# Kernel tuning notes

Hardware: AMD Instinct MI355X
Metric: run time of the kernel (lower is better)

Reference implementation:

```python
import jax, jax.numpy as jnp
import numpy as np

B, C, H, W = 32, 3, 512, 512
EPS = 1e-8


def _radius_bins(h, w):
    cy, cx = h // 2, w // 2
    y = jnp.arange(h, dtype=jnp.float32) - cy
    x = jnp.arange(w, dtype=jnp.float32) - cx
    radius = jnp.sqrt(y[:, None] ** 2 + x[None, :] ** 2)  # [H, W]
    max_r = min(cy, cx)
    bins = jnp.floor(radius).astype(jnp.int32)
    # pixels with radius >= max_r fall outside all bins in the original loop;
    # route them to a dummy overflow bin that we drop afterwards.
    bins = jnp.where(bins < max_r, bins, max_r)
    return bins.reshape(-1), max_r


def _psd(x):
    f = jnp.fft.fft2(x)                  # over last two dims, like torch.fft.fft2
    psd = jnp.abs(f) ** 2
    return jnp.log(psd + EPS)            # log_power=True


def _radial_average(psd):
    b, c, h, w = psd.shape
    bins, max_r = _radius_bins(h, w)     # [H*W], static
    data = psd.reshape(b * c, h * w).T   # [H*W, B*C]
    sums = jax.ops.segment_sum(data, bins, num_segments=max_r + 1)
    counts = jax.ops.segment_sum(jnp.ones((h * w,), psd.dtype), bins,
                                 num_segments=max_r + 1)
    avg = jnp.where(counts[:, None] > 0, sums / counts[:, None], 0.0)
    avg = avg[:max_r]                    # drop overflow bin -> [max_r, B*C]
    return avg.T.reshape(b, c, max_r)


def setup_inputs() -> dict:
    key = jax.random.key(0)
    k1, k2 = jax.random.split(key)
    predicted = jax.random.normal(k1, (B, C, H, W), dtype=jnp.float32)
    target = jax.random.normal(k2, (B, C, H, W), dtype=jnp.float32)
    return {"predicted": predicted, "target": target}


def reference(predicted, target):
    pred_rad = _radial_average(_psd(predicted))
    targ_rad = _radial_average(_psd(target))
    return jnp.mean(jnp.abs(pred_rad - targ_rad))  # l1, reduction='mean'
```

## Files before the change

kernel.cpp:

```cpp
#include <hip/hip_runtime.h>
#include <math.h>

#define HH 512
#define WW 512
#define IMG (HH*WW)
#define NIMG_PER 96
#define NIMG 192
#define NBIN 256
#define EPSV 1e-8f
#define LN2F 0.69314718055994530942f

#define CSTR 264
#define IMGC (512*CSTR)
#define NT16 17
#define SLOT 575

typedef float v2f  __attribute__((ext_vector_type(2)));
typedef _Float16 h2f __attribute__((ext_vector_type(2)));

__device__ __forceinline__ int drev(int s) {
    return ((s & 7) << 6) | (s & 56) | (s >> 6);
}
__device__ __forceinline__ int fsw(int a) { return a + (a >> 3); }

__device__ __forceinline__ v2f cmul(v2f a, v2f b) {
    return (v2f){a.x, a.x} * b + (v2f){a.y, a.y} * (v2f){-b.y, b.x};
}
__device__ __forceinline__ v2f cni(v2f a) { return (v2f){a.y, -a.x}; }

__device__ __forceinline__ v2f h2tof(unsigned int u) {
    h2f h = __builtin_bit_cast(h2f, u);
    return (v2f){(float)h.x, (float)h.y};
}
__device__ __forceinline__ unsigned int ftoh2(v2f v) {
    return __builtin_bit_cast(unsigned int, __builtin_amdgcn_cvt_pkrtz(v.x, v.y));
}

__device__ __forceinline__ void wsync() {
    asm volatile("" ::: "memory");
    __builtin_amdgcn_wave_barrier();
    asm volatile("" ::: "memory");
}

__device__ __forceinline__ void bfly8(v2f x[8]) {
    const float R = 0.70710678118654752440f;
    v2f t0=x[0]+x[4], t4=x[0]-x[4];
    v2f t1=x[1]+x[5], t5=x[1]-x[5];
    v2f t2=x[2]+x[6], t6=x[2]-x[6];
    v2f t3=x[3]+x[7], t7=x[3]-x[7];
    v2f u0=t0+t2, u2=t0-t2;
    v2f u1=t1+t3, u3=t1-t3;
    x[0]=u0+u1; x[4]=u0-u1;
    { v2f n3 = cni(u3); x[2]=u2+n3; x[6]=u2-n3; }
    v2f s1 = (v2f){R, R} * ((v2f){t5.x, t5.y} + (v2f){t5.y, -t5.x});
    v2f s2 = cni(t6);
    v2f s3 = (v2f){R, R} * ((v2f){t7.y, -t7.x} - (v2f){t7.x, t7.y});
    v2f v0=t4+s2, v2_=t4-s2;
    v2f v1=s1+s3, v3=s1-s3;
    x[1]=v0+v1; x[5]=v0-v1;
    { v2f m3 = cni(v3); x[3]=v2_+m3; x[7]=v2_-m3; }
}

__device__ __forceinline__ void twiddle7(v2f* x, float ang) {
    const float sn = __sinf(ang), cs = __cosf(ang);
    const v2f w1 = (v2f){cs, sn};
    const v2f w2 = cmul(w1, w1);
    const v2f w3 = cmul(w2, w1);
    const v2f w4 = cmul(w2, w2);
    const v2f w5 = cmul(w2, w3);
    const v2f w6 = cmul(w3, w3);
    const v2f w7 = cmul(w3, w4);
    x[1]=cmul(x[1],w1); x[2]=cmul(x[2],w2); x[3]=cmul(x[3],w3);
    x[4]=cmul(x[4],w4); x[5]=cmul(x[5],w5); x[6]=cmul(x[6],w6);
    x[7]=cmul(x[7],w7);
}

__global__ __launch_bounds__(512) void rowfft_kernel(
    const float* __restrict__ pred, const float* __restrict__ targ,
    unsigned int* __restrict__ out, int img_base)
{
    __shared__ v2f sd[8*SLOT];
    const int t    = threadIdx.x;
    const int lane = t & 63;
    const int w    = t >> 6;

    const int pb = blockIdx.x;
    const int li = blockIdx.y;
    const int g  = img_base + li;
    const float* img = (g < NIMG_PER) ? (pred + (size_t)g * IMG)
                                      : (targ + (size_t)(g - NIMG_PER) * IMG);
    const float* rowA = img + (size_t)(pb*16 + 2*w) * WW + lane;
    const float* rowB = rowA + WW;

    v2f* p = sd + w * SLOT;
    v2f x[8];
    const int i = lane;

    #pragma unroll
    for (int j = 0; j < 8; ++j)
        x[j] = (v2f){rowA[64*j], rowB[64*j]};
    bfly8(x);
    twiddle7(x, -0.012271846303085130f * (float)i);
    {
        v2f* q = p + fsw(i);
        #pragma unroll
        for (int j = 0; j < 8; ++j) q[72*j] = x[j];
    }
    wsync();

    {
        v2f* q = p + 72*(i >> 3) + (i & 7);
        #pragma unroll
        for (int j = 0; j < 8; ++j) x[j] = q[9*j];
        bfly8(x);
        twiddle7(x, -0.098174770424681038f * (float)(i & 7));
        #pragma unroll
        for (int j = 0; j < 8; ++j) q[9*j] = x[j];
    }
    wsync();

    {
        v2f* q = p + 9*i;
        #pragma unroll
        for (int j = 0; j < 8; ++j) x[j] = q[j];
        bfly8(x);
        #pragma unroll
        for (int j = 0; j < 8; ++j) q[j] = x[j];
    }
    wsync();

    unsigned int* dstA = out + (size_t)li * IMGC + (size_t)(pb*16 + 2*w) * CSTR;
    unsigned int* dstB = dstA + CSTR;
    #pragma unroll
    for (int it = 0; it < 5; ++it) {
        const int k = it*64 + lane;
        if (k <= 256) {
            const v2f P = p[fsw(drev(k))];
            const v2f Q = p[fsw(drev((512 - k) & 511))];
            const v2f Fa = (v2f){0.5f, 0.5f} * (P + (v2f){Q.x, -Q.y});
            const v2f Fb = (v2f){0.5f, 0.5f} * ((v2f){P.y, -P.x} + (v2f){Q.y, Q.x});
            dstA[k] = ftoh2(Fa);
            dstB[k] = ftoh2(Fb);
        } else if (k < CSTR) {
            dstA[k] = 0u;
            dstB[k] = 0u;
        }
    }
}

__global__ __launch_bounds__(512) void colfft_kernel(
    const unsigned int* __restrict__ in, float* __restrict__ bins2, int img_base)
{
    __shared__ unsigned int sd[16*SLOT];
    __shared__ float bs[4*257];
    const int t    = threadIdx.x;
    const int lane = t & 63;
    const int w    = t >> 6;

    for (int id = t; id < 4*257; id += 512) bs[id] = 0.0f;

    const int li = blockIdx.y;
    const int x0 = blockIdx.x * 16;
    {
        const int y0 = t >> 2;
        const int c  = t & 3;
        int cb = x0 + 4*c;
        if (cb > CSTR - 4) cb = CSTR - 4;
        const uint4* gsrc = (const uint4*)(in + (size_t)li * IMGC
                                              + (size_t)y0 * CSTR + cb);
        unsigned int* d0 = sd + (4*c + 0)*SLOT + fsw(y0);
        unsigned int* d1 = d0 + SLOT;
        unsigned int* d2 = d1 + SLOT;
        unsigned int* d3 = d2 + SLOT;
        #pragma unroll
        for (int it = 0; it < 4; ++it) {
            const uint4 v = gsrc[(size_t)it * 128 * (CSTR/4)];
            d0[144*it] = v.x; d1[144*it] = v.y;
            d2[144*it] = v.z; d3[144*it] = v.w;
        }
    }
    __syncthreads();

    unsigned int* pA = sd + (2*w)     * SLOT;
    unsigned int* pB = sd + (2*w + 1) * SLOT;
    v2f a[8], b[8];
    const int i = lane;

    {
        unsigned int* qA = pA + fsw(i);
        unsigned int* qB = pB + fsw(i);
        #pragma unroll
        for (int j = 0; j < 8; ++j) { a[j] = h2tof(qA[72*j]); b[j] = h2tof(qB[72*j]); }
        bfly8(a); bfly8(b);
        const float ang = -0.012271846303085130f * (float)i;
        const float sn = __sinf(ang), cs = __cosf(ang);
        const v2f w1 = (v2f){cs, sn};
        const v2f w2 = cmul(w1,w1), w3 = cmul(w2,w1), w4 = cmul(w2,w2);
        const v2f w5 = cmul(w2,w3), w6 = cmul(w3,w3), w7 = cmul(w3,w4);
        a[1]=cmul(a[1],w1); b[1]=cmul(b[1],w1);
        a[2]=cmul(a[2],w2); b[2]=cmul(b[2],w2);
        a[3]=cmul(a[3],w3); b[3]=cmul(b[3],w3);
        a[4]=cmul(a[4],w4); b[4]=cmul(b[4],w4);
        a[5]=cmul(a[5],w5); b[5]=cmul(b[5],w5);
        a[6]=cmul(a[6],w6); b[6]=cmul(b[6],w6);
        a[7]=cmul(a[7],w7); b[7]=cmul(b[7],w7);
        #pragma unroll
        for (int j = 0; j < 8; ++j) { qA[72*j] = ftoh2(a[j]); qB[72*j] = ftoh2(b[j]); }
    }
    wsync();

    {
        const int off = 72*(i >> 3) + (i & 7);
        unsigned int* qA = pA + off;
        unsigned int* qB = pB + off;
        #pragma unroll
        for (int j = 0; j < 8; ++j) { a[j] = h2tof(qA[9*j]); b[j] = h2tof(qB[9*j]); }
        bfly8(a); bfly8(b);
        const float ang = -0.098174770424681038f * (float)(i & 7);
        const float sn = __sinf(ang), cs = __cosf(ang);
        const v2f w1 = (v2f){cs, sn};
        const v2f w2 = cmul(w1,w1), w3 = cmul(w2,w1), w4 = cmul(w2,w2);
        const v2f w5 = cmul(w2,w3), w6 = cmul(w3,w3), w7 = cmul(w3,w4);
        a[1]=cmul(a[1],w1); b[1]=cmul(b[1],w1);
        a[2]=cmul(a[2],w2); b[2]=cmul(b[2],w2);
        a[3]=cmul(a[3],w3); b[3]=cmul(b[3],w3);
        a[4]=cmul(a[4],w4); b[4]=cmul(b[4],w4);
        a[5]=cmul(a[5],w5); b[5]=cmul(b[5],w5);
        a[6]=cmul(a[6],w6); b[6]=cmul(b[6],w6);
        a[7]=cmul(a[7],w7); b[7]=cmul(b[7],w7);
        #pragma unroll
        for (int j = 0; j < 8; ++j) { qA[9*j] = ftoh2(a[j]); qB[9*j] = ftoh2(b[j]); }
    }
    wsync();

    {
        unsigned int* qA = pA + 9*i;
        unsigned int* qB = pB + 9*i;
        #pragma unroll
        for (int j = 0; j < 8; ++j) { a[j] = h2tof(qA[j]); b[j] = h2tof(qB[j]); }
        bfly8(a); bfly8(b);
        #pragma unroll
        for (int j = 0; j < 8; ++j) { qA[j] = ftoh2(a[j]); qB[j] = ftoh2(b[j]); }
    }
    wsync();

    {
        const int h   = lane;
        const int kxA = x0 + 2*w;
        const int kxB = kxA + 1;
        const bool vA = (kxA <= 256), vB = (kxB <= 256);
        const float sA = (kxA == 0 || kxA == 256) ? 0.5f : 1.0f;
        const float sB = (kxB == 256) ? 0.5f : 1.0f;
        const float dxA = (float)((kxA - 256) * (kxA - 256));
        const float dxB = (float)((kxB - 256) * (kxB - 256));
        float* bsw = bs + (w & 3) * 257;
        const int off = fsw(8*(h & 7) + (h >> 3));
        unsigned int* qA = pA + off;
        unsigned int* qB = pB + off;
        float dyf = (float)(8*h - 256);

        float accA = 0.0f, accB = 0.0f;
        int pbA = 1000, pbB = 1000;
        #pragma unroll
        for (int j = 0; j < 8; ++j) {
            const v2f va = h2tof(qA[72*j]);
            const v2f vb = h2tof(qB[72*j]);
            const float la = __log2f(fmaf(va.x, va.x, fmaf(va.y, va.y, EPSV)));
            const float lb = __log2f(fmaf(vb.x, vb.x, fmaf(vb.y, vb.y, EPSV)));
            const int bA = (int)sqrtf(fmaf(dyf, dyf, dxA));
            const int bB = (int)sqrtf(fmaf(dyf, dyf, dxB));
            dyf += 1.0f;
            if (bA != pbA) {
                if (pbA < NBIN && vA) atomicAdd(&bsw[pbA], accA * sA);
                pbA = bA; accA = la;
            } else accA += la;
            if (bB != pbB) {
                if (pbB < NBIN && vB) atomicAdd(&bsw[pbB], accB * sB);
                pbB = bB; accB = lb;
            } else accB += lb;
        }
        if (pbA < NBIN && vA) atomicAdd(&bsw[pbA], accA * sA);
        if (pbB < NBIN && vB) atomicAdd(&bsw[pbB], accB * sB);
    }
    __syncthreads();

    if (t < NBIN) {
        float v = 0.0f;
        #pragma unroll
        for (int r = 0; r < 4; ++r) v += bs[r*257 + t];
        bins2[((size_t)blockIdx.x * NIMG + (img_base + li)) * NBIN + t] = 2.0f * v;
    }
}

__global__ __launch_bounds__(256) void reduce_kernel(
    const float* __restrict__ bins2, float* __restrict__ bins)
{
    const int li = blockIdx.x;
    const int t  = threadIdx.x;
    float s = 0.0f;
    #pragma unroll
    for (int tile = 0; tile < NT16; ++tile)
        s += bins2[((size_t)tile * NIMG + li) * NBIN + t];
    bins[(size_t)li * NBIN + t] = s;
}

__global__ __launch_bounds__(256) void counts_kernel(float* __restrict__ cnt)
{
    __shared__ float c[NBIN];
    const int t = threadIdx.x;
    c[t] = 0.0f;
    __syncthreads();

    const int base = blockIdx.x * 4096;
    #pragma unroll
    for (int i = 0; i < 16; ++i) {
        const int id = base + i * 256 + t;
        const int y = id >> 9, xx = id & 511;
        const int dy = y - 256, dx = xx - 256;
        const int b  = (int)sqrtf((float)(dy*dy + dx*dx));
        if (b < NBIN) atomicAdd(&c[b], 1.0f);
    }
    __syncthreads();
    if (c[t] != 0.0f) atomicAdd(&cnt[t], c[t]);
}

__global__ __launch_bounds__(256) void finalize_kernel(
    const float* __restrict__ bins, const float* __restrict__ cnt,
    float* __restrict__ out)
{
    __shared__ float red[256];
    const int t = threadIdx.x;

    float acc = 0.0f;
    for (int id = t; id < NIMG_PER * NBIN; id += 256) {
        const int i = id >> 8;
        const int r = id & 255;
        const float d = fabsf(bins[(size_t)i * NBIN + r]
                            - bins[(size_t)(NIMG_PER + i) * NBIN + r]);
        acc += d / cnt[r];
    }
    red[t] = acc;
    __syncthreads();
    for (int w = 128; w > 0; w >>= 1) {
        if (t < w) red[t] += red[t + w];
        __syncthreads();
    }
    if (t == 0) out[0] = red[0] * (LN2F / (float)(NIMG_PER * NBIN));
}

extern "C" void kernel_launch(void* const* d_in, const int* in_sizes, int n_in,
                              void* d_out, int out_size, void* d_ws, size_t ws_size,
                              hipStream_t stream)
{
    const float* pred = (const float*)d_in[0];
    const float* targ = (const float*)d_in[1];
    float* out = (float*)d_out;

    char* ws = (char*)d_ws;
    float* cnt   = (float*)ws;
    float* bins  = cnt + NBIN;
    float* bins2 = bins + (size_t)NIMG * NBIN;
    const size_t fixed_f = NBIN + (size_t)NIMG*NBIN + (size_t)NT16*NIMG*NBIN;
    const size_t off = (fixed_f*sizeof(float) + 255) & ~(size_t)255;
    unsigned int* cbuf = (unsigned int*)(ws + off);

    const size_t per_img = (size_t)IMGC * sizeof(unsigned int);
    size_t avail = (ws_size > off) ? (ws_size - off) : 0;
    int chunk = (int)(avail / per_img);
    if (chunk > NIMG) chunk = NIMG;
    if (chunk < 1) chunk = 1;

    hipMemsetAsync(cnt, 0, NBIN * sizeof(float), stream);
    counts_kernel<<<dim3(64), dim3(256), 0, stream>>>(cnt);

    for (int base = 0; base < NIMG; base += chunk) {
        const int n = (NIMG - base < chunk) ? (NIMG - base) : chunk;
        dim3 gA(HH / 16, n), gB(NT16, n);
        rowfft_kernel<<<gA, dim3(512), 0, stream>>>(pred, targ, cbuf, base);
        colfft_kernel<<<gB, dim3(512), 0, stream>>>(cbuf, bins2, base);
    }

    reduce_kernel<<<dim3(NIMG), dim3(256), 0, stream>>>(bins2, bins);
    finalize_kernel<<<dim3(1), dim3(256), 0, stream>>>(bins, cnt, out);
}
```

Measured before the change: 212.9 us.

## Software-pipeline row and column FFT stages across image chunks in combo kernel

```diff
diff --git a/kernel.cpp b/kernel.cpp
--- a/kernel.cpp
+++ b/kernel.cpp
@@ -14,6 +14,10 @@
 #define IMGC (512*CSTR)
 #define NT16 17
 #define SLOT 575
+#define SMEM_BYTES 40960
+
+#define CHUNK 48
+#define NCHUNK 4
 
 typedef float v2f  __attribute__((ext_vector_type(2)));
 typedef _Float16 h2f __attribute__((ext_vector_type(2)));
@@ -75,18 +79,15 @@
     x[7]=cmul(x[7],w7);
 }
 
-__global__ __launch_bounds__(512) void rowfft_kernel(
-    const float* __restrict__ pred, const float* __restrict__ targ,
-    unsigned int* __restrict__ out, int img_base)
-{
-    __shared__ v2f sd[8*SLOT];
+__device__ __forceinline__ void rowfft_body(
+    char* smem, const float* __restrict__ pred, const float* __restrict__ targ,
+    unsigned int* __restrict__ out, int g, int pb)
+{
+    v2f* sd = (v2f*)smem;
     const int t    = threadIdx.x;
     const int lane = t & 63;
     const int w    = t >> 6;
 
-    const int pb = blockIdx.x;
-    const int li = blockIdx.y;
-    const int g  = img_base + li;
     const float* img = (g < NIMG_PER) ? (pred + (size_t)g * IMG)
                                       : (targ + (size_t)(g - NIMG_PER) * IMG);
     const float* rowA = img + (size_t)(pb*16 + 2*w) * WW + lane;
@@ -129,7 +130,7 @@
     }
     wsync();
 
-    unsigned int* dstA = out + (size_t)li * IMGC + (size_t)(pb*16 + 2*w) * CSTR;
+    unsigned int* dstA = out + (size_t)g * IMGC + (size_t)(pb*16 + 2*w) * CSTR;
     unsigned int* dstB = dstA + CSTR;
     #pragma unroll
     for (int it = 0; it < 5; ++it) {
@@ -148,25 +149,25 @@
     }
 }
 
-__global__ __launch_bounds__(512) void colfft_kernel(
-    const unsigned int* __restrict__ in, float* __restrict__ bins2, int img_base)
-{
-    __shared__ unsigned int sd[16*SLOT];
-    __shared__ float bs[4*257];
+__device__ __forceinline__ void colfft_body(
+    char* smem, const unsigned int* __restrict__ in,
+    float* __restrict__ bins2, int g, int tile)
+{
+    unsigned int* sd = (unsigned int*)smem;
+    float* bs = (float*)(smem + 16*SLOT*sizeof(unsigned int));
     const int t    = threadIdx.x;
     const int lane = t & 63;
     const int w    = t >> 6;
 
     for (int id = t; id < 4*257; id += 512) bs[id] = 0.0f;
 
-    const int li = blockIdx.y;
-    const int x0 = blockIdx.x * 16;
+    const int x0 = tile * 16;
     {
         const int y0 = t >> 2;
         const int c  = t & 3;
         int cb = x0 + 4*c;
         if (cb > CSTR - 4) cb = CSTR - 4;
-        const uint4* gsrc = (const uint4*)(in + (size_t)li * IMGC
+        const uint4* gsrc = (const uint4*)(in + (size_t)g * IMGC
                                               + (size_t)y0 * CSTR + cb);
         unsigned int* d0 = sd + (4*c + 0)*SLOT + fsw(y0);
         unsigned int* d1 = d0 + SLOT;
@@ -288,8 +289,35 @@
         float v = 0.0f;
         #pragma unroll
         for (int r = 0; r < 4; ++r) v += bs[r*257 + t];
-        bins2[((size_t)blockIdx.x * NIMG + (img_base + li)) * NBIN + t] = 2.0f * v;
-    }
+        bins2[((size_t)tile * NIMG + g) * NBIN + t] = 2.0f * v;
+    }
+}
+
+__global__ __launch_bounds__(512) void rowfft_kernel(
+    const float* __restrict__ pred, const float* __restrict__ targ,
+    unsigned int* __restrict__ out, int img_base)
+{
+    extern __shared__ char smem[];
+    rowfft_body(smem, pred, targ, out, img_base + blockIdx.y, blockIdx.x);
+}
+
+__global__ __launch_bounds__(512) void colfft_kernel(
+    const unsigned int* __restrict__ in, float* __restrict__ bins2, int img_base)
+{
+    extern __shared__ char smem[];
+    colfft_body(smem, in, bins2, img_base + blockIdx.y, blockIdx.x);
+}
+
+__global__ __launch_bounds__(512) void combo_kernel(
+    const float* __restrict__ pred, const float* __restrict__ targ,
+    unsigned int* __restrict__ cbuf, float* __restrict__ bins2,
+    int row_base, int col_base)
+{
+    extern __shared__ char smem[];
+    if (blockIdx.x < 32)
+        rowfft_body(smem, pred, targ, cbuf, row_base + blockIdx.y, blockIdx.x);
+    else
+        colfft_body(smem, cbuf, bins2, col_base + blockIdx.y, blockIdx.x - 32);
 }
 
 __global__ __launch_bounds__(256) void reduce_kernel(
@@ -364,21 +392,17 @@
     const size_t off = (fixed_f*sizeof(float) + 255) & ~(size_t)255;
     unsigned int* cbuf = (unsigned int*)(ws + off);
 
-    const size_t per_img = (size_t)IMGC * sizeof(unsigned int);
-    size_t avail = (ws_size > off) ? (ws_size - off) : 0;
-    int chunk = (int)(avail / per_img);
-    if (chunk > NIMG) chunk = NIMG;
-    if (chunk < 1) chunk = 1;
-
     hipMemsetAsync(cnt, 0, NBIN * sizeof(float), stream);
     counts_kernel<<<dim3(64), dim3(256), 0, stream>>>(cnt);
 
-    for (int base = 0; base < NIMG; base += chunk) {
-        const int n = (NIMG - base < chunk) ? (NIMG - base) : chunk;
-        dim3 gA(HH / 16, n), gB(NT16, n);
-        rowfft_kernel<<<gA, dim3(512), 0, stream>>>(pred, targ, cbuf, base);
-        colfft_kernel<<<gB, dim3(512), 0, stream>>>(cbuf, bins2, base);
-    }
+    rowfft_kernel<<<dim3(32, CHUNK), dim3(512), SMEM_BYTES, stream>>>(
+        pred, targ, cbuf, 0);
+    for (int k = 1; k < NCHUNK; ++k) {
+        combo_kernel<<<dim3(32 + NT16, CHUNK), dim3(512), SMEM_BYTES, stream>>>(
+            pred, targ, cbuf, bins2, k*CHUNK, (k-1)*CHUNK);
+    }
+    colfft_kernel<<<dim3(NT16, CHUNK), dim3(512), SMEM_BYTES, stream>>>(
+        cbuf, bins2, (NCHUNK-1)*CHUNK);
 
     reduce_kernel<<<dim3(NIMG), dim3(256), 0, stream>>>(bins2, bins);
     finalize_kernel<<<dim3(1), dim3(256), 0, stream>>>(bins, cnt, out);
```

Measured after the change: 285.3 us. 34.0% more time.
